# Optimization experiments

Measured on AMD Instinct MI355X. Metric: run time of the kernel, lower is better.

Reference implementation:

```python
import jax, jax.numpy as jnp
import numpy as np

N, IN_XC, IN_YC, OUTC, H, W = 8, 512, 256, 256, 96, 96
C2 = OUTC // 2  # 128
K = 3
NUM_LAT = K * K // 2 + 1  # 5


def conv2d(x, w, b=None, pad=0):
    out = jax.lax.conv_general_dilated(
        x, w, window_strides=(1, 1), padding=[(pad, pad), (pad, pad)],
        dimension_numbers=('NCHW', 'OIHW', 'NCHW'))
    if b is not None:
        out = out + b[None, :, None, None]
    return out


def patches3x3(x):
    # torch nn.Unfold(3, padding=1) taps, ordered (kh, kw) row-major -> [N,C,9,H,W]
    n, c, h, w = x.shape
    xp = jnp.pad(x, ((0, 0), (0, 0), (1, 1), (1, 1)))
    cols = [xp[:, :, i:i + h, j:j + w] for i in range(3) for j in range(3)]
    return jnp.stack(cols, axis=2)


def pool_to_3x3(x):
    # AdaptiveAvgPool2d(3) with H,W divisible by 3 == mean over equal bins
    n, c, h, w = x.shape
    return x.reshape(n, c, 3, h // 3, 3, w // 3).mean(axis=(3, 5))


def setup_inputs() -> dict:
    key = jax.random.key(0)
    ks = jax.random.split(key, 24)
    g = lambda i, shape, s=0.05: (jax.random.normal(ks[i], shape, dtype=jnp.float32) * s)
    return {
        'x': jax.random.normal(ks[0], (N, IN_XC, H, W), dtype=jnp.float32),
        'y': jax.random.normal(ks[1], (N, IN_YC, H, W), dtype=jnp.float32),
        # SDFM.down_input: 1x1 conv in_xC -> out_C
        'w_down': g(2, (OUTC, IN_XC, 1, 1)), 'b_down': g(3, (OUTC,)),
        # channel-attention MLP over 3x3 pooled grid
        'w_ce': g(4, (NUM_LAT, K * K)), 'w_gd': g(5, (K * K, NUM_LAT)),
        'bn_g': jnp.ones((C2,), jnp.float32), 'bn_b': jnp.zeros((C2,), jnp.float32),
        # gernerate_kernel_channel: 1x1 conv mid_in_yC -> mid_in_xC (both 128)
        'w_kc': g(6, (C2, C2, 1, 1)), 'b_kc': g(7, (C2,)),
        # gernerate_kernel_spatial: 3x3 conv C2->C2 then 1x1 conv C2->9
        'w_ks1': g(8, (C2, C2, 3, 3)), 'b_ks1': g(9, (C2,)),
        'w_ks2': g(10, (K * K, C2, 1, 1)), 'b_ks2': g(11, (K * K,)),
        # spatial-attention convs (bias=False)
        'w_sp1': g(12, (1, C2, 3, 3)), 'w_sp': g(13, (1, 2, 3, 3)),
        # branch fuse: 3x3 conv out_C -> out_C
        'w_fb': g(14, (OUTC, 2 * C2, 3, 3)), 'b_fb': g(15, (OUTC,)),
        # SDFM.fuse (BasicConv_PRelu): 3x3 conv 2*out_C -> out_C, BN(eval), PReLU
        'w_fuse': g(16, (OUTC, 2 * OUTC, 3, 3)),
        'bn2_g': jnp.ones((OUTC,), jnp.float32), 'bn2_b': jnp.zeros((OUTC,), jnp.float32),
        'prelu_a': jnp.full((OUTC,), 0.25, jnp.float32),
    }


def reference(x, y, w_down, b_down, w_ce, w_gd, bn_g, bn_b, w_kc, b_kc,
              w_ks1, b_ks1, w_ks2, b_ks2, w_sp1, w_sp, w_fb, b_fb,
              w_fuse, bn2_g, bn2_b, prelu_a):
    # SDFM.down_input
    x = conv2d(x, w_down, b_down, pad=0)          # [N, 256, H, W]
    n, c, h, w = x.shape
    c2 = c // 2
    x1, x2 = x[:, :c2], x[:, c2:]                 # [N,128,H,W] each
    y1, y2 = y[:, :c2], y[:, c2:]

    # --- channel branch: per-(sample,channel) dynamic 3x3 depthwise kernel ---
    gl = pool_to_3x3(x1).reshape(n, c2, K * K)    # [N,128,9]
    att = gl @ w_ce.T                              # ce (no bias) -> [N,128,5]
    att = att * bn_g[None, :, None] + bn_b[None, :, None]  # BN1d eval (rm=0, rv=1)
    att = jax.nn.relu(att)
    att = jax.nn.sigmoid(att @ w_gd.T)            # [N,128,9]

    kc = conv2d(pool_to_3x3(y1), w_kc, b_kc, pad=0)  # [N,128,3,3]
    kc = kc.reshape(n, c2, K * K) * att           # [N,128,9]
    # grouped conv (groups = N*C/2) == per-sample depthwise dynamic conv
    channel_after = jnp.einsum('nckhw,nck->nchw', patches3x3(x1), kc)

    # --- spatial branch: per-pixel dynamic 3x3 kernel ---
    ks = conv2d(conv2d(y2, w_ks1, b_ks1, pad=1), w_ks2, b_ks2, pad=0)  # [N,9,H,W]

    ksp = conv2d(x2, w_sp1, None, pad=1)          # [N,1,H,W]
    p = patches3x3(ksp).reshape(n, K * K, h, w)   # [N,9,H,W]
    avg = p.mean(axis=1, keepdims=True)
    mx = p.max(axis=1, keepdims=True)
    sp = jax.nn.sigmoid(conv2d(jnp.concatenate([avg, mx], axis=1), w_sp, None, pad=1))  # [N,1,H,W]

    kernel_after = (ks * sp).transpose(0, 2, 3, 1)[..., None]  # [N,H,W,9,1]

    # faithful replication of the original quirky reshape of unfold output:
    # [N, C2*9, H*W] -> [N, H, W, C2, 9]
    unfold_x = patches3x3(x2).reshape(n, c2 * K * K, h * w).reshape(n, h, w, c2, K * K)
    spatial_after = jnp.matmul(unfold_x, kernel_after)[..., 0]  # [N,H,W,C2]
    spatial_after = spatial_after.transpose(0, 3, 1, 2)          # [N,C2,H,W]

    result = jnp.concatenate([channel_after, spatial_after], axis=1)  # [N,256,H,W]
    r1 = conv2d(result, w_fb, b_fb, pad=1)        # branch fuse 3x3

    # SDFM.fuse: BasicConv_PRelu = conv3x3 (no bias) + BN(eval, rm=0,rv=1) + PReLU
    o = conv2d(jnp.concatenate([x, r1], axis=1), w_fuse, None, pad=1)
    o = o * bn2_g[None, :, None, None] + bn2_b[None, :, None, None]
    o = jnp.where(o >= 0, o, prelu_a[None, :, None, None] * o)
    return o
```

## Files before the change

kernel.cpp:

```cpp
#include <hip/hip_runtime.h>
#include <hip/hip_bf16.h>
#include <math.h>

#define HW 9216
#define IMG 96

typedef __bf16 bf16x8 __attribute__((ext_vector_type(8)));
typedef float  f32x4  __attribute__((ext_vector_type(4)));

__device__ __forceinline__ void gload16(const void* g, void* l) {
    __builtin_amdgcn_global_load_lds((const unsigned int*)g, (unsigned int*)l, 16, 0, 0);
}

#define WAITVN(N) asm volatile("s_waitcnt vmcnt(" #N ")" ::: "memory")
#define BARX()    { asm volatile("" ::: "memory"); __builtin_amdgcn_s_barrier(); asm volatile("" ::: "memory"); }

__global__ __launch_bounds__(256) void nchw2nhwc_kernel(
    const float* __restrict__ src, long n_stride_src,
    __hip_bfloat16* __restrict__ dst, int dst_stride)
{
    __shared__ float tile[32][65];
    const int px0 = blockIdx.x * 64;
    const int c0  = blockIdx.y * 32;
    const int n   = blockIdx.z;
    const int tid = threadIdx.x;
    const int tx = tid & 63, ty = tid >> 6;
    #pragma unroll
    for (int i = 0; i < 8; ++i)
        tile[ty + i * 4][tx] = src[n * n_stride_src + (long)(c0 + ty + i * 4) * HW + px0 + tx];
    __syncthreads();
    const int ci = tid & 31, pxl = tid >> 5;
    #pragma unroll
    for (int j = 0; j < 8; ++j) {
        int px = pxl + j * 8;
        dst[((long)n * HW + px0 + px) * dst_stride + c0 + ci] = __float2bfloat16(tile[ci][px]);
    }
}

__global__ __launch_bounds__(256) void wconv_kernel(
    const float* __restrict__ src, __hip_bfloat16* __restrict__ dst,
    int cout, int cin, int taps)
{
    int idx = blockIdx.x * 256 + threadIdx.x;
    if (idx >= cout * cin) return;
    int co = idx / cin, ci = idx % cin;
    for (int t = 0; t < taps; ++t)
        dst[((long)t * cout + co) * cin + ci] = __float2bfloat16(src[(long)idx * taps + t]);
}

template<int CIN, int TAPS, bool SPLIT>
__global__ __launch_bounds__(512, 1) void mfma_conv(
    const __hip_bfloat16* __restrict__ in_a,
    const __hip_bfloat16* __restrict__ in_b,
    const __hip_bfloat16* __restrict__ w_t,
    const float* __restrict__ bias,
    float* __restrict__ out_nchw, long nchw_nstride,
    __hip_bfloat16* __restrict__ out_nhwc, int nhwc_stride,
    int cout,
    const float* __restrict__ bng, const float* __restrict__ bnb,
    const float* __restrict__ pra,
    const __hip_bfloat16* __restrict__ zeropage)
{
    constexpr int ROWS = (TAPS == 9) ? 10 : 8;
    constexpr int COLS = (TAPS == 9) ? 98 : 96;
    constexpr int HOFF = (TAPS == 9) ? 1 : 0;
    constexpr int PSTR = SPLIT ? 256 : CIN;
    constexpr int NSEG_IN = ROWS * COLS * 4;
    constexpr int NSEG_W  = TAPS * 32 * 4;
    constexpr int IN_BYTES = NSEG_IN * 16;
    constexpr int BUF = IN_BYTES + NSEG_W * 16;
    constexpr int NCHUNK = CIN / 32;
    constexpr int FULL_IN = NSEG_IN / 512;
    constexpr int IN_TAIL = NSEG_IN % 512;
    constexpr int FULL_W  = NSEG_W / 512;
    constexpr int W_TAIL  = NSEG_W % 512;
    constexpr int IT_IN = FULL_IN + (IN_TAIL ? 1 : 0);
    constexpr int IT_W  = FULL_W + (W_TAIL ? 1 : 0);

    extern __shared__ __align__(16) char lds[];

    const int h0   = blockIdx.x * 8;
    const int cob  = blockIdx.y * 32;
    const int n    = blockIdx.z;
    const int tid  = threadIdx.x;
    const int lane = tid & 63;
    const int wave = tid >> 6;
    const int l16  = lane & 15, lg = lane >> 4;

    const long dAB = SPLIT ? ((const char*)in_b - (const char*)in_a - 448) : 0;

    const char* inptr[IT_IN];
    int inval[IT_IN];
    #pragma unroll
    for (int t = 0; t < IT_IN; ++t) {
        int seg = tid + t * 512;
        int s2 = (seg < NSEG_IN) ? seg : 0;
        int pix = s2 >> 2, qp = s2 & 3;
        int r = pix / COLS, c = pix % COLS;
        int h = h0 + r - HOFF, w = c - HOFF;
        int q = qp ^ ((c >> 1) & 3);
        bool valid = (h >= 0 && h < IMG && w >= 0 && w < IMG);
        inptr[t] = valid
            ? (const char*)(in_a + ((long)n * HW + h * IMG + w) * PSTR + q * 8)
            : (const char*)zeropage;
        inval[t] = valid ? 1 : 0;
    }
    const char* wptr[IT_W];
    #pragma unroll
    for (int t = 0; t < IT_W; ++t) {
        int seg = tid + t * 512;
        int s2 = (seg < NSEG_W) ? seg : 0;
        int tap = s2 >> 7, rem = s2 & 127;
        int co = rem >> 2, qp = rem & 3;
        int q = qp ^ ((co >> 1) & 3);
        wptr[t] = (const char*)(w_t + ((long)tap * cout + cob + co) * CIN + q * 8);
    }

    auto stage = [&](int bb, long adv) {
        char* ib = lds + bb * BUF;
        char* wb = ib + IN_BYTES;
        #pragma unroll
        for (int t = 0; t < FULL_IN; ++t) {
            gload16(inptr[t], ib + (tid + t * 512) * 16);
            if (inval[t]) inptr[t] += adv;
        }
        if (IN_TAIL) {
            if (tid < IN_TAIL) {
                gload16(inptr[IT_IN - 1], ib + (tid + FULL_IN * 512) * 16);
                if (inval[IT_IN - 1]) inptr[IT_IN - 1] += adv;
            }
        }
        #pragma unroll
        for (int t = 0; t < FULL_W; ++t) {
            gload16(wptr[t], wb + (tid + t * 512) * 16);
            wptr[t] += 64;
        }
        if (W_TAIL) {
            if (tid < W_TAIL) {
                gload16(wptr[IT_W - 1], wb + (tid + FULL_W * 512) * 16);
                wptr[IT_W - 1] += 64;
            }
        }
    };

    f32x4 acc[2][6];
    #pragma unroll
    for (int m = 0; m < 2; ++m)
        #pragma unroll
        for (int nf = 0; nf < 6; ++nf) acc[m][nf] = (f32x4){0.f, 0.f, 0.f, 0.f};

    const int qa = lg ^ ((l16 >> 1) & 3);
    const int a_off = l16 * 64 + qa * 16;

    stage(0, 64);
    WAITVN(0); BARX();

    for (int ch = 0; ch < NCHUNK; ++ch) {
        if (ch + 1 < NCHUNK) {
            long adv = (SPLIT && (ch + 1) == 7) ? dAB : 64;
            stage((ch + 1) & 1, adv);
            if constexpr (TAPS == 9) {
                if (wave < 2) { WAITVN(11); } else if (wave < 6) { WAITVN(10); } else { WAITVN(9); }
            } else {
                if (wave < 2) { WAITVN(7); } else { WAITVN(6); }
            }
        } else {
            WAITVN(0);
        }
        BARX();

        const char* ib = lds + (ch & 1) * BUF;
        const char* wb = ib + IN_BYTES;
        __builtin_amdgcn_s_setprio(1);
        #pragma unroll
        for (int tap = 0; tap < TAPS; ++tap) {
            const int g = (TAPS == 9) ? tap / 3 : 0;
            const int kx = (TAPS == 9) ? tap % 3 : 0;
            bf16x8 a0 = *(const bf16x8*)(wb + tap * 2048 + a_off);
            bf16x8 a1 = *(const bf16x8*)(wb + tap * 2048 + 1024 + a_off);
            #pragma unroll
            for (int nf = 0; nf < 6; ++nf) {
                const int c = nf * 16 + l16 + kx;
                const int qb = lg ^ ((c >> 1) & 3);
                bf16x8 b = *(const bf16x8*)(ib + ((wave + g) * COLS + c) * 64 + qb * 16);
                acc[0][nf] = __builtin_amdgcn_mfma_f32_16x16x32_bf16(a0, b, acc[0][nf], 0, 0, 0);
                acc[1][nf] = __builtin_amdgcn_mfma_f32_16x16x32_bf16(a1, b, acc[1][nf], 0, 0, 0);
            }
        }
        __builtin_amdgcn_s_setprio(0);
        BARX();
    }

    const int hrow = h0 + wave;
    #pragma unroll
    for (int m = 0; m < 2; ++m) {
        const int co = cob + m * 16 + lg * 4;
        float bs[4], g4[4], b4[4], p4[4];
        #pragma unroll
        for (int r = 0; r < 4; ++r) bs[r] = bias ? bias[co + r] : 0.f;
        if (bng) {
            #pragma unroll
            for (int r = 0; r < 4; ++r) { g4[r] = bng[co + r]; b4[r] = bnb[co + r]; p4[r] = pra[co + r]; }
        }
        #pragma unroll
        for (int nf = 0; nf < 6; ++nf) {
            const int wcol = nf * 16 + l16;
            const long px = (long)hrow * IMG + wcol;
            float v[4];
            #pragma unroll
            for (int r = 0; r < 4; ++r) {
                v[r] = acc[m][nf][r] + bs[r];
                if (bng) {
                    v[r] = v[r] * g4[r] + b4[r];
                    v[r] = (v[r] >= 0.f) ? v[r] : p4[r] * v[r];
                }
            }
            if (out_nchw) {
                #pragma unroll
                for (int r = 0; r < 4; ++r)
                    out_nchw[(long)n * nchw_nstride + (long)(co + r) * HW + px] = v[r];
            }
            if (out_nhwc) {
                union { __hip_bfloat16 h[4]; uint2 u; } pk;
                #pragma unroll
                for (int r = 0; r < 4; ++r) pk.h[r] = __float2bfloat16(v[r]);
                *reinterpret_cast<uint2*>(&out_nhwc[((long)n * HW + px) * nhwc_stride + co]) = pk.u;
            }
        }
    }
}

__global__ __launch_bounds__(256) void pool_kernel(
    const float* __restrict__ xd, const float* __restrict__ y,
    float* __restrict__ gl, float* __restrict__ py)
{
    const int c = blockIdx.x, n = blockIdx.y, which = blockIdx.z;
    const int tid = threadIdx.x;
    const float* src = (which == 0) ? (xd + ((long)n * 256 + c) * HW)
                                    : (y  + ((long)n * 256 + c) * HW);
    float local[9];
    #pragma unroll
    for (int k = 0; k < 9; ++k) local[k] = 0.f;
    for (int i = tid; i < HW; i += 256) {
        int h = i / 96, w = i % 96;
        local[(h / 32) * 3 + (w / 32)] += src[i];
    }
    __shared__ float red[9][4];
    const int wv = tid >> 6, lane = tid & 63;
    #pragma unroll
    for (int k = 0; k < 9; ++k) {
        float v = local[k];
        for (int off = 32; off > 0; off >>= 1) v += __shfl_down(v, off, 64);
        if (lane == 0) red[k][wv] = v;
    }
    __syncthreads();
    if (tid < 9) {
        float s = (red[tid][0] + red[tid][1] + red[tid][2] + red[tid][3]) * (1.f / 1024.f);
        float* dst = (which == 0) ? gl : py;
        dst[((long)n * 128 + c) * 9 + tid] = s;
    }
}

__global__ __launch_bounds__(128) void attkc_kernel(
    const float* __restrict__ gl, const float* __restrict__ py,
    const float* __restrict__ w_ce, const float* __restrict__ w_gd,
    const float* __restrict__ bng, const float* __restrict__ bnb,
    const float* __restrict__ w_kc, const float* __restrict__ b_kc,
    float* __restrict__ kc)
{
    const int n = blockIdx.x, c = threadIdx.x;
    __shared__ float py_s[128][9];
    #pragma unroll
    for (int k = 0; k < 9; ++k) py_s[c][k] = py[((long)n * 128 + c) * 9 + k];
    __syncthreads();
    float g[9];
    #pragma unroll
    for (int k = 0; k < 9; ++k) g[k] = gl[((long)n * 128 + c) * 9 + k];
    float t[5];
    #pragma unroll
    for (int l = 0; l < 5; ++l) {
        float s = 0.f;
        #pragma unroll
        for (int k = 0; k < 9; ++k) s += g[k] * w_ce[l * 9 + k];
        s = s * bng[c] + bnb[c];
        t[l] = s > 0.f ? s : 0.f;
    }
    float att[9];
    #pragma unroll
    for (int k = 0; k < 9; ++k) {
        float s = 0.f;
        #pragma unroll
        for (int l = 0; l < 5; ++l) s += t[l] * w_gd[k * 5 + l];
        att[k] = 1.f / (1.f + expf(-s));
    }
    float kc0[9];
    float bk = b_kc[c];
    #pragma unroll
    for (int k = 0; k < 9; ++k) kc0[k] = bk;
    for (int c2 = 0; c2 < 128; ++c2) {
        float wv = w_kc[c * 128 + c2];
        #pragma unroll
        for (int k = 0; k < 9; ++k) kc0[k] += wv * py_s[c2][k];
    }
    #pragma unroll
    for (int k = 0; k < 9; ++k)
        kc[((long)n * 128 + c) * 9 + k] = kc0[k] * att[k];
}

__global__ __launch_bounds__(256) void channel_nhwc_kernel(
    const __hip_bfloat16* __restrict__ catx, const float* __restrict__ kc,
    __hip_bfloat16* __restrict__ catfb)
{
    const int h  = blockIdx.x;
    const int n  = blockIdx.y;
    const int cg = (threadIdx.x & 15) * 8;
    const int w0 = threadIdx.x >> 4;
    float k9[8][9];
    #pragma unroll
    for (int j = 0; j < 8; ++j)
        #pragma unroll
        for (int t = 0; t < 9; ++t) k9[j][t] = kc[((long)n * 128 + cg + j) * 9 + t];
    const long pbase = (long)n * HW;
    for (int it = 0; it < 6; ++it) {
        const int w = w0 + it * 16;
        float acc[8];
        #pragma unroll
        for (int j = 0; j < 8; ++j) acc[j] = 0.f;
        #pragma unroll
        for (int ky = 0; ky < 3; ++ky) {
            const int hh = h + ky - 1;
            if (hh < 0 || hh >= IMG) continue;
            #pragma unroll
            for (int kx = 0; kx < 3; ++kx) {
                const int ww = w + kx - 1;
                if (ww < 0 || ww >= IMG) continue;
                bf16x8 v = *reinterpret_cast<const bf16x8*>(
                    &catx[(pbase + hh * IMG + ww) * 256 + cg]);
                #pragma unroll
                for (int j = 0; j < 8; ++j)
                    acc[j] += k9[j][ky * 3 + kx] * (float)v[j];
            }
        }
        union { __hip_bfloat16 hh[8]; uint4 u; } pk;
        #pragma unroll
        for (int j = 0; j < 8; ++j) pk.hh[j] = __float2bfloat16(acc[j]);
        *reinterpret_cast<uint4*>(&catfb[(pbase + h * IMG + w) * 256 + cg]) = pk.u;
    }
}

__global__ __launch_bounds__(256) void ks_kernel(
    const float* __restrict__ ksmid, const float* __restrict__ w_ks2,
    const float* __restrict__ b_ks2, float* __restrict__ ks)
{
    __shared__ float w_s[9 * 128];
    const int tid = threadIdx.x;
    for (int i = tid; i < 1152; i += 256) w_s[i] = w_ks2[i];
    __syncthreads();
    const int p = blockIdx.x * 256 + tid;
    const int n = blockIdx.y;
    float acc[9];
    #pragma unroll
    for (int k = 0; k < 9; ++k) acc[k] = b_ks2[k];
    for (int c = 0; c < 128; ++c) {
        float v = ksmid[((long)n * 128 + c) * HW + p];
        #pragma unroll
        for (int k = 0; k < 9; ++k) acc[k] += w_s[k * 128 + c] * v;
    }
    #pragma unroll
    for (int k = 0; k < 9; ++k) ks[((long)n * 9 + k) * HW + p] = acc[k];
}

__global__ __launch_bounds__(256) void ksp_nhwc_kernel(
    const __hip_bfloat16* __restrict__ catx, const float* __restrict__ w_sp1,
    float* __restrict__ ksp)
{
    __shared__ float w_s[9][128];
    const int tid = threadIdx.x;
    for (int i = tid; i < 1152; i += 256) {
        int ci = i / 9, tap = i % 9;
        w_s[tap][ci] = w_sp1[i];
    }
    __syncthreads();
    const int p = blockIdx.x * 256 + tid;
    const int n = blockIdx.y;
    const int h = p / 96, w = p % 96;
    const long pbase = (long)n * HW;
    float acc = 0.f;
    #pragma unroll
    for (int ky = 0; ky < 3; ++ky) {
        const int hh = h + ky - 1;
        if (hh < 0 || hh >= IMG) continue;
        #pragma unroll
        for (int kx = 0; kx < 3; ++kx) {
            const int ww = w + kx - 1;
            if (ww < 0 || ww >= IMG) continue;
            const int tap = ky * 3 + kx;
            const __hip_bfloat16* row = &catx[(pbase + hh * IMG + ww) * 256 + 128];
            #pragma unroll
            for (int vq = 0; vq < 16; ++vq) {
                bf16x8 v = *reinterpret_cast<const bf16x8*>(&row[vq * 8]);
                #pragma unroll
                for (int j = 0; j < 8; ++j)
                    acc += w_s[tap][vq * 8 + j] * (float)v[j];
            }
        }
    }
    ksp[pbase + p] = acc;
}

__global__ __launch_bounds__(256) void sp_kernel(
    const float* __restrict__ ksp, const float* __restrict__ w_sp,
    float* __restrict__ sp)
{
    const int p = blockIdx.x * 256 + threadIdx.x;
    const int n = blockIdx.y;
    const int h = p / 96, w = p % 96;
    const float* kp = ksp + (long)n * HW;
    float acc = 0.f;
    #pragma unroll
    for (int dy = 0; dy < 3; ++dy)
        #pragma unroll
        for (int dx = 0; dx < 3; ++dx) {
            int hh = h + dy - 1, ww = w + dx - 1;
            if (hh < 0 || hh >= 96 || ww < 0 || ww >= 96) continue;
            float s = 0.f, m = -1e30f;
            #pragma unroll
            for (int iy = 0; iy < 3; ++iy)
                #pragma unroll
                for (int ix = 0; ix < 3; ++ix) {
                    int h2 = hh + iy - 1, w2 = ww + ix - 1;
                    float v = (h2 >= 0 && h2 < 96 && w2 >= 0 && w2 < 96) ? kp[h2 * 96 + w2] : 0.f;
                    s += v; m = fmaxf(m, v);
                }
            acc += w_sp[dy * 3 + dx] * (s * (1.f / 9.f)) + w_sp[9 + dy * 3 + dx] * m;
        }
    sp[(long)n * HW + p] = 1.f / (1.f + expf(-acc));
}

__global__ __launch_bounds__(256) void spatial_kernel(
    const float* __restrict__ xd, const float* __restrict__ ks,
    const float* __restrict__ sp, __hip_bfloat16* __restrict__ catfb)
{
    const int cc = blockIdx.x;
    const int n  = blockIdx.y;
    const int tid = threadIdx.x;
    __shared__ float plane[HW];
    const float* src = xd + ((long)n * 256 + 128 + cc) * HW;
    for (int i = tid; i < HW / 4; i += 256)
        *reinterpret_cast<float4*>(&plane[i * 4]) = *reinterpret_cast<const float4*>(&src[i * 4]);
    __syncthreads();
    const int c  = tid & 127;
    const int pr = tid >> 7;
    const int c9 = c * 9;
    for (int j = 0; j < 36; ++j) {
        const int pl = pr + j * 2;
        const int p  = cc * 72 + pl;
        float spv = sp[(long)n * HW + p];
        float kv[9];
        #pragma unroll
        for (int k = 0; k < 9; ++k) kv[k] = ks[((long)n * 9 + k) * HW + p] * spv;
        const int base = pl * 1152 + c9;
        int kk0 = base / 9216;
        int r20 = base - kk0 * 9216;
        int h20 = r20 / 96;
        int w20 = r20 - h20 * 96;
        float acc = 0.f;
        #pragma unroll
        for (int k = 0; k < 9; ++k) {
            int kk = kk0, h2 = h20, w2 = w20 + k;
            if (w2 >= 96) { h2 += 1; w2 -= 96; }
            if (h2 >= 96) { kk += 1; h2 -= 96; }
            int hh = h2 + kk / 3 - 1;
            int ww = w2 + kk % 3 - 1;
            float v = (hh >= 0 && hh < 96 && ww >= 0 && ww < 96) ? plane[hh * 96 + ww] : 0.f;
            acc += v * kv[k];
        }
        catfb[((long)n * HW + p) * 256 + 128 + c] = __float2bfloat16(acc);
    }
}

extern "C" void kernel_launch(void* const* d_in, const int* in_sizes, int n_in,
                              void* d_out, int out_size, void* d_ws, size_t ws_size,
                              hipStream_t stream)
{
    const float* x      = (const float*)d_in[0];
    const float* y      = (const float*)d_in[1];
    const float* w_down = (const float*)d_in[2];
    const float* b_down = (const float*)d_in[3];
    const float* w_ce   = (const float*)d_in[4];
    const float* w_gd   = (const float*)d_in[5];
    const float* bn_g   = (const float*)d_in[6];
    const float* bn_b   = (const float*)d_in[7];
    const float* w_kc   = (const float*)d_in[8];
    const float* b_kc   = (const float*)d_in[9];
    const float* w_ks1  = (const float*)d_in[10];
    const float* b_ks1  = (const float*)d_in[11];
    const float* w_ks2  = (const float*)d_in[12];
    const float* b_ks2  = (const float*)d_in[13];
    const float* w_sp1  = (const float*)d_in[14];
    const float* w_sp   = (const float*)d_in[15];
    const float* w_fb   = (const float*)d_in[16];
    const float* b_fb   = (const float*)d_in[17];
    const float* w_fuse = (const float*)d_in[18];
    const float* bn2_g  = (const float*)d_in[19];
    const float* bn2_b  = (const float*)d_in[20];
    const float* prelu  = (const float*)d_in[21];
    float* out = (float*)d_out;
    char* ws = (char*)d_ws;

    const long HWl = HW;
    float* xd = (float*)ws;                               ws += 8L * 256 * HWl * 4;
    char* region2 = ws;                                   ws += 8L * HWl * 512 * 2;
    __hip_bfloat16* x_t    = (__hip_bfloat16*)region2;
    __hip_bfloat16* cat_r1 = (__hip_bfloat16*)region2;
    float*          ksmid  = (float*)region2;
    __hip_bfloat16* catfb  = (__hip_bfloat16*)(region2 + 8L * HWl * 256 * 2);
    __hip_bfloat16* cat_x  = (__hip_bfloat16*)ws;         ws += 8L * HWl * 256 * 2;
    __hip_bfloat16* y2t    = (__hip_bfloat16*)ws;         ws += 8L * HWl * 128 * 2;
    __hip_bfloat16* wdown_bf = (__hip_bfloat16*)ws;       ws += 1L * 256 * 512 * 2;
    __hip_bfloat16* wks1_bf  = (__hip_bfloat16*)ws;       ws += 9L * 128 * 128 * 2;
    __hip_bfloat16* wfb_bf   = (__hip_bfloat16*)ws;       ws += 9L * 256 * 256 * 2;
    __hip_bfloat16* wfuse_bf = (__hip_bfloat16*)ws;       ws += 9L * 256 * 512 * 2;
    float* ks   = (float*)ws;  ws += 8L * 9 * HWl * 4;
    float* ksp  = (float*)ws;  ws += 8L * HWl * 4;
    float* spb  = (float*)ws;  ws += 8L * HWl * 4;
    float* gl   = (float*)ws;  ws += 8L * 128 * 9 * 4;
    float* py   = (float*)ws;  ws += 8L * 128 * 9 * 4;
    float* kc   = (float*)ws;  ws += 8L * 128 * 9 * 4;
    __hip_bfloat16* zp = (__hip_bfloat16*)ws;  ws += 256;

    (void)hipMemsetAsync((void*)zp, 0, 256, stream);

    wconv_kernel<<<dim3(512), 256, 0, stream>>>(w_down, wdown_bf, 256, 512, 1);
    wconv_kernel<<<dim3(64),  256, 0, stream>>>(w_ks1,  wks1_bf,  128, 128, 9);
    wconv_kernel<<<dim3(256), 256, 0, stream>>>(w_fb,   wfb_bf,   256, 256, 9);
    wconv_kernel<<<dim3(512), 256, 0, stream>>>(w_fuse, wfuse_bf, 256, 512, 9);

    nchw2nhwc_kernel<<<dim3(144, 16, 8), 256, 0, stream>>>(x, 512L * HWl, x_t, 512);
    mfma_conv<512, 1, false><<<dim3(12, 8, 8), 512, 102400, stream>>>(
        x_t, nullptr, wdown_bf, b_down, xd, 256L * HWl, cat_x, 256, 256,
        nullptr, nullptr, nullptr, zp);

    nchw2nhwc_kernel<<<dim3(144, 4, 8), 256, 0, stream>>>(y + 128L * HWl, 256L * HWl, y2t, 128);

    pool_kernel<<<dim3(128, 8, 2), 256, 0, stream>>>(xd, y, gl, py);
    attkc_kernel<<<dim3(8), 128, 0, stream>>>(gl, py, w_ce, w_gd, bn_g, bn_b, w_kc, b_kc, kc);

    mfma_conv<128, 9, false><<<dim3(12, 4, 8), 512, 162304, stream>>>(
        y2t, nullptr, wks1_bf, b_ks1, ksmid, 128L * HWl, nullptr, 0, 128,
        nullptr, nullptr, nullptr, zp);
    ks_kernel<<<dim3(36, 8), 256, 0, stream>>>(ksmid, w_ks2, b_ks2, ks);

    ksp_nhwc_kernel<<<dim3(36, 8), 256, 0, stream>>>(cat_x, w_sp1, ksp);
    sp_kernel<<<dim3(36, 8), 256, 0, stream>>>(ksp, w_sp, spb);

    spatial_kernel<<<dim3(128, 8), 256, 0, stream>>>(xd, ks, spb, catfb);
    channel_nhwc_kernel<<<dim3(96, 8), 256, 0, stream>>>(cat_x, kc, catfb);

    mfma_conv<256, 9, false><<<dim3(12, 8, 8), 512, 162304, stream>>>(
        catfb, nullptr, wfb_bf, b_fb, nullptr, 0, cat_r1, 256, 256,
        nullptr, nullptr, nullptr, zp);

    mfma_conv<512, 9, true><<<dim3(12, 8, 8), 512, 162304, stream>>>(
        cat_x, cat_r1, wfuse_bf, nullptr, out, 256L * HWl, nullptr, 0, 256,
        bn2_g, bn2_b, prelu, zp);
}
```

Before: 671.6 us.

## Switch conv kernel to 32x32x16 MFMA with smaller blocks and two-per-CU occupancy

The implicit-GEMM conv kernel moves from 16x16x32 to 32x32x16 bf16 MFMA. Each block now handles 4 output rows by 64 output channels with 256 threads, and launch bounds allow two blocks per CU. The LDS layout changes from the XOR-swizzled layout to a grouped-by-8-pixel slot layout, and the K chunk shrinks to 16 or 32 channels, so the pipeline has more stages with smaller stages. The goals are more reuse per MFMA, fewer LDS bytes per block, and overlap between co-resident blocks. The risks are more halo rows per output row, more barriers, and possible LDS bank conflicts without the swizzle.

```diff
diff --git a/kernel.cpp b/kernel.cpp
--- a/kernel.cpp
+++ b/kernel.cpp
@@ -7,6 +7,7 @@
 
 typedef __bf16 bf16x8 __attribute__((ext_vector_type(8)));
 typedef float  f32x4  __attribute__((ext_vector_type(4)));
+typedef float  f32x16 __attribute__((ext_vector_type(16)));
 
 __device__ __forceinline__ void gload16(const void* g, void* l) {
     __builtin_amdgcn_global_load_lds((const unsigned int*)g, (unsigned int*)l, 16, 0, 0);
@@ -49,7 +50,7 @@
 }
 
 template<int CIN, int TAPS, bool SPLIT>
-__global__ __launch_bounds__(512, 1) void mfma_conv(
+__global__ __launch_bounds__(256, 2) void mfma_conv(
     const __hip_bfloat16* __restrict__ in_a,
     const __hip_bfloat16* __restrict__ in_b,
     const __hip_bfloat16* __restrict__ w_t,
@@ -61,45 +62,58 @@
     const float* __restrict__ pra,
     const __hip_bfloat16* __restrict__ zeropage)
 {
-    constexpr int ROWS = (TAPS == 9) ? 10 : 8;
+    constexpr int KSTEPS = (TAPS == 1) ? 2 : 1;
+    constexpr int QD     = 2 * KSTEPS;
+    constexpr int CICH   = 16 * KSTEPS;
+    constexpr int ROWS = (TAPS == 9) ? 6 : 4;
     constexpr int COLS = (TAPS == 9) ? 98 : 96;
     constexpr int HOFF = (TAPS == 9) ? 1 : 0;
     constexpr int PSTR = SPLIT ? 256 : CIN;
-    constexpr int NSEG_IN = ROWS * COLS * 4;
-    constexpr int NSEG_W  = TAPS * 32 * 4;
-    constexpr int IN_BYTES = NSEG_IN * 16;
-    constexpr int BUF = IN_BYTES + NSEG_W * 16;
-    constexpr int NCHUNK = CIN / 32;
-    constexpr int FULL_IN = NSEG_IN / 512;
-    constexpr int IN_TAIL = NSEG_IN % 512;
-    constexpr int FULL_W  = NSEG_W / 512;
-    constexpr int W_TAIL  = NSEG_W % 512;
-    constexpr int IT_IN = FULL_IN + (IN_TAIL ? 1 : 0);
-    constexpr int IT_W  = FULL_W + (W_TAIL ? 1 : 0);
+    constexpr int GP        = (COLS + 7) / 8;
+    constexpr int ROWSLOTS  = GP * 8 * QD;
+    constexpr int IN_SLOTS  = ROWS * ROWSLOTS;
+    constexpr int IN_BYTES  = IN_SLOTS * 16;
+    constexpr int WTAP      = 64 * QD;
+    constexpr int W_SLOTS   = TAPS * WTAP;
+    constexpr int BUF       = IN_BYTES + W_SLOTS * 16;
+    constexpr int NCHUNK    = CIN / CICH;
+    constexpr int FULL_IN = IN_SLOTS / 256;
+    constexpr int IN_TAIL = IN_SLOTS % 256;
+    constexpr int IT_IN   = FULL_IN + (IN_TAIL ? 1 : 0);
+    constexpr int FULL_W  = W_SLOTS / 256;
+    constexpr int W_TAIL  = W_SLOTS % 256;
+    constexpr int IT_W    = FULL_W + (W_TAIL ? 1 : 0);
+    constexpr int CROSS   = 256 / CICH;
+    constexpr long ADV    = 2 * CICH;
 
     extern __shared__ __align__(16) char lds[];
 
-    const int h0   = blockIdx.x * 8;
-    const int cob  = blockIdx.y * 32;
+    const int h0   = blockIdx.x * 4;
+    const int cob  = blockIdx.y * 64;
     const int n    = blockIdx.z;
     const int tid  = threadIdx.x;
     const int lane = tid & 63;
     const int wave = tid >> 6;
-    const int l16  = lane & 15, lg = lane >> 4;
-
-    const long dAB = SPLIT ? ((const char*)in_b - (const char*)in_a - 448) : 0;
+    const int l31  = lane & 31;
+    const int lq   = lane >> 5;
+    const int g3   = l31 >> 3, c7 = l31 & 7;
+
+    const long dAB = SPLIT ? ((const char*)in_b - (const char*)in_a - (CROSS - 1) * ADV) : 0;
 
     const char* inptr[IT_IN];
     int inval[IT_IN];
     #pragma unroll
     for (int t = 0; t < IT_IN; ++t) {
-        int seg = tid + t * 512;
-        int s2 = (seg < NSEG_IN) ? seg : 0;
-        int pix = s2 >> 2, qp = s2 & 3;
-        int r = pix / COLS, c = pix % COLS;
-        int h = h0 + r - HOFF, w = c - HOFF;
-        int q = qp ^ ((c >> 1) & 3);
-        bool valid = (h >= 0 && h < IMG && w >= 0 && w < IMG);
+        int seg = tid + t * 256;
+        int s2 = (seg < IN_SLOTS) ? seg : 0;
+        int r  = s2 / ROWSLOTS;
+        int sl = s2 - r * ROWSLOTS;
+        int g8 = sl / (8 * QD);
+        int rem = sl - g8 * 8 * QD;
+        int q  = rem >> 3, p7 = rem & 7;
+        int px = g8 * 8 + p7;
+        int h = h0 + r - HOFF, w = px - HOFF;
+        bool valid = (px < COLS) && (h >= 0 && h < IMG && w >= 0 && w < IMG);
         inptr[t] = valid
             ? (const char*)(in_a + ((long)n * HW + h * IMG + w) * PSTR + q * 8)
             : (const char*)zeropage;
@@ -108,11 +122,14 @@
     const char* wptr[IT_W];
     #pragma unroll
     for (int t = 0; t < IT_W; ++t) {
-        int seg = tid + t * 512;
-        int s2 = (seg < NSEG_W) ? seg : 0;
-        int tap = s2 >> 7, rem = s2 & 127;
-        int co = rem >> 2, qp = rem & 3;
-        int q = qp ^ ((co >> 1) & 3);
+        int seg = tid + t * 256;
+        int s2 = (seg < W_SLOTS) ? seg : 0;
+        int tap = s2 / WTAP;
+        int sl  = s2 - tap * WTAP;
+        int g8 = sl / (8 * QD);
+        int rem = sl - g8 * 8 * QD;
+        int q  = rem >> 3, p7 = rem & 7;
+        int co = g8 * 8 + p7;
         wptr[t] = (const char*)(w_t + ((long)tap * cout + cob + co) * CIN + q * 8);
     }
 
@@ -121,48 +138,47 @@
         char* wb = ib + IN_BYTES;
         #pragma unroll
         for (int t = 0; t < FULL_IN; ++t) {
-            gload16(inptr[t], ib + (tid + t * 512) * 16);
+            gload16(inptr[t], ib + (tid + t * 256) * 16);
             if (inval[t]) inptr[t] += adv;
         }
         if (IN_TAIL) {
             if (tid < IN_TAIL) {
-                gload16(inptr[IT_IN - 1], ib + (tid + FULL_IN * 512) * 16);
+                gload16(inptr[IT_IN - 1], ib + (tid + FULL_IN * 256) * 16);
                 if (inval[IT_IN - 1]) inptr[IT_IN - 1] += adv;
             }
         }
         #pragma unroll
         for (int t = 0; t < FULL_W; ++t) {
-            gload16(wptr[t], wb + (tid + t * 512) * 16);
-            wptr[t] += 64;
+            gload16(wptr[t], wb + (tid + t * 256) * 16);
+            wptr[t] += ADV;
         }
         if (W_TAIL) {
             if (tid < W_TAIL) {
-                gload16(wptr[IT_W - 1], wb + (tid + FULL_W * 512) * 16);
-                wptr[IT_W - 1] += 64;
+                gload16(wptr[IT_W - 1], wb + (tid + FULL_W * 256) * 16);
+                wptr[IT_W - 1] += ADV;
             }
         }
     };
 
-    f32x4 acc[2][6];
-    #pragma unroll
-    for (int m = 0; m < 2; ++m)
-        #pragma unroll
-        for (int nf = 0; nf < 6; ++nf) acc[m][nf] = (f32x4){0.f, 0.f, 0.f, 0.f};
-
-    const int qa = lg ^ ((l16 >> 1) & 3);
-    const int a_off = l16 * 64 + qa * 16;
-
-    stage(0, 64);
+    f32x16 acc[2][3];
+    #pragma unroll
+    for (int mf = 0; mf < 2; ++mf)
+        #pragma unroll
+        for (int nf = 0; nf < 3; ++nf)
+            #pragma unroll
+            for (int e = 0; e < 16; ++e) acc[mf][nf][e] = 0.f;
+
+    stage(0, ADV);
     WAITVN(0); BARX();
 
     for (int ch = 0; ch < NCHUNK; ++ch) {
         if (ch + 1 < NCHUNK) {
-            long adv = (SPLIT && (ch + 1) == 7) ? dAB : 64;
+            long adv = (SPLIT && (ch + 2) == CROSS) ? dAB : ADV;
             stage((ch + 1) & 1, adv);
             if constexpr (TAPS == 9) {
-                if (wave < 2) { WAITVN(11); } else if (wave < 6) { WAITVN(10); } else { WAITVN(9); }
+                if (wave < 2) { WAITVN(10); } else { WAITVN(9); }
             } else {
-                if (wave < 2) { WAITVN(7); } else { WAITVN(6); }
+                WAITVN(7);
             }
         } else {
             WAITVN(0);
@@ -171,60 +187,68 @@
 
         const char* ib = lds + (ch & 1) * BUF;
         const char* wb = ib + IN_BYTES;
+        const int rowbase = wave;
         __builtin_amdgcn_s_setprio(1);
         #pragma unroll
         for (int tap = 0; tap < TAPS; ++tap) {
-            const int g = (TAPS == 9) ? tap / 3 : 0;
+            const int g  = (TAPS == 9) ? tap / 3 : 0;
             const int kx = (TAPS == 9) ? tap % 3 : 0;
-            bf16x8 a0 = *(const bf16x8*)(wb + tap * 2048 + a_off);
-            bf16x8 a1 = *(const bf16x8*)(wb + tap * 2048 + 1024 + a_off);
-            #pragma unroll
-            for (int nf = 0; nf < 6; ++nf) {
-                const int c = nf * 16 + l16 + kx;
-                const int qb = lg ^ ((c >> 1) & 3);
-                bf16x8 b = *(const bf16x8*)(ib + ((wave + g) * COLS + c) * 64 + qb * 16);
-                acc[0][nf] = __builtin_amdgcn_mfma_f32_16x16x32_bf16(a0, b, acc[0][nf], 0, 0, 0);
-                acc[1][nf] = __builtin_amdgcn_mfma_f32_16x16x32_bf16(a1, b, acc[1][nf], 0, 0, 0);
+            #pragma unroll
+            for (int ks = 0; ks < KSTEPS; ++ks) {
+                const int q = ks * 2 + lq;
+                bf16x8 a0 = *(const bf16x8*)(wb + (tap * WTAP + ((g3)     * QD + q) * 8 + c7) * 16);
+                bf16x8 a1 = *(const bf16x8*)(wb + (tap * WTAP + ((4 + g3) * QD + q) * 8 + c7) * 16);
+                #pragma unroll
+                for (int nf = 0; nf < 3; ++nf) {
+                    const int px = nf * 32 + kx + l31;
+                    const int slot = ((px >> 3) * QD + q) * 8 + (px & 7);
+                    bf16x8 b = *(const bf16x8*)(ib + ((rowbase + g) * ROWSLOTS + slot) * 16);
+                    acc[0][nf] = __builtin_amdgcn_mfma_f32_32x32x16_bf16(a0, b, acc[0][nf], 0, 0, 0);
+                    acc[1][nf] = __builtin_amdgcn_mfma_f32_32x32x16_bf16(a1, b, acc[1][nf], 0, 0, 0);
+                }
             }
         }
         __builtin_amdgcn_s_setprio(0);
         BARX();
     }
 
-    const int hrow = h0 + wave;
-    #pragma unroll
-    for (int m = 0; m < 2; ++m) {
-        const int co = cob + m * 16 + lg * 4;
-        float bs[4], g4[4], b4[4], p4[4];
-        #pragma unroll
-        for (int r = 0; r < 4; ++r) bs[r] = bias ? bias[co + r] : 0.f;
-        if (bng) {
-            #pragma unroll
-            for (int r = 0; r < 4; ++r) { g4[r] = bng[co + r]; b4[r] = bnb[co + r]; p4[r] = pra[co + r]; }
-        }
-        #pragma unroll
-        for (int nf = 0; nf < 6; ++nf) {
-            const int wcol = nf * 16 + l16;
-            const long px = (long)hrow * IMG + wcol;
-            float v[4];
-            #pragma unroll
-            for (int r = 0; r < 4; ++r) {
-                v[r] = acc[m][nf][r] + bs[r];
-                if (bng) {
-                    v[r] = v[r] * g4[r] + b4[r];
-                    v[r] = (v[r] >= 0.f) ? v[r] : p4[r] * v[r];
+    const int row = h0 + wave;
+    #pragma unroll
+    for (int mf = 0; mf < 2; ++mf) {
+        #pragma unroll
+        for (int rr = 0; rr < 4; ++rr) {
+            const int co = cob + mf * 32 + rr * 8 + lq * 4;
+            float bs[4], g4[4], b4[4], p4[4];
+            #pragma unroll
+            for (int j = 0; j < 4; ++j) bs[j] = bias ? bias[co + j] : 0.f;
+            if (bng) {
+                #pragma unroll
+                for (int j = 0; j < 4; ++j) { g4[j] = bng[co + j]; b4[j] = bnb[co + j]; p4[j] = pra[co + j]; }
+            }
+            #pragma unroll
+            for (int nf = 0; nf < 3; ++nf) {
+                const int px = nf * 32 + l31;
+                const long pix = (long)row * IMG + px;
+                float v[4];
+                #pragma unroll
+                for (int j = 0; j < 4; ++j) {
+                    v[j] = acc[mf][nf][rr * 4 + j] + bs[j];
+                    if (bng) {
+                        v[j] = v[j] * g4[j] + b4[j];
+                        v[j] = (v[j] >= 0.f) ? v[j] : p4[j] * v[j];
+                    }
                 }
-            }
-            if (out_nchw) {
-                #pragma unroll
-                for (int r = 0; r < 4; ++r)
-                    out_nchw[(long)n * nchw_nstride + (long)(co + r) * HW + px] = v[r];
-            }
-            if (out_nhwc) {
-                union { __hip_bfloat16 h[4]; uint2 u; } pk;
-                #pragma unroll
-                for (int r = 0; r < 4; ++r) pk.h[r] = __float2bfloat16(v[r]);
-                *reinterpret_cast<uint2*>(&out_nhwc[((long)n * HW + px) * nhwc_stride + co]) = pk.u;
+                if (out_nchw) {
+                    #pragma unroll
+                    for (int j = 0; j < 4; ++j)
+                        out_nchw[(long)n * nchw_nstride + (long)(co + j) * HW + pix] = v[j];
+                }
+                if (out_nhwc) {
+                    union { __hip_bfloat16 h[4]; uint2 u; } pk;
+                    #pragma unroll
+                    for (int j = 0; j < 4; ++j) pk.h[j] = __float2bfloat16(v[j]);
+                    *reinterpret_cast<uint2*>(&out_nhwc[((long)n * HW + pix) * nhwc_stride + co]) = pk.u;
+                }
             }
         }
     }
@@ -537,7 +561,7 @@
     wconv_kernel<<<dim3(512), 256, 0, stream>>>(w_fuse, wfuse_bf, 256, 512, 9);
 
     nchw2nhwc_kernel<<<dim3(144, 16, 8), 256, 0, stream>>>(x, 512L * HWl, x_t, 512);
-    mfma_conv<512, 1, false><<<dim3(12, 8, 8), 512, 102400, stream>>>(
+    mfma_conv<512, 1, false><<<dim3(24, 4, 8), 256, 57344, stream>>>(
         x_t, nullptr, wdown_bf, b_down, xd, 256L * HWl, cat_x, 256, 256,
         nullptr, nullptr, nullptr, zp);
 
@@ -546,7 +570,7 @@
     pool_kernel<<<dim3(128, 8, 2), 256, 0, stream>>>(xd, y, gl, py);
     attkc_kernel<<<dim3(8), 128, 0, stream>>>(gl, py, w_ce, w_gd, bn_g, bn_b, w_kc, b_kc, kc);
 
-    mfma_conv<128, 9, false><<<dim3(12, 4, 8), 512, 162304, stream>>>(
+    mfma_conv<128, 9, false><<<dim3(24, 2, 8), 256, 76800, stream>>>(
         y2t, nullptr, wks1_bf, b_ks1, ksmid, 128L * HWl, nullptr, 0, 128,
         nullptr, nullptr, nullptr, zp);
     ks_kernel<<<dim3(36, 8), 256, 0, stream>>>(ksmid, w_ks2, b_ks2, ks);
@@ -557,11 +581,11 @@
     spatial_kernel<<<dim3(128, 8), 256, 0, stream>>>(xd, ks, spb, catfb);
     channel_nhwc_kernel<<<dim3(96, 8), 256, 0, stream>>>(cat_x, kc, catfb);
 
-    mfma_conv<256, 9, false><<<dim3(12, 8, 8), 512, 162304, stream>>>(
+    mfma_conv<256, 9, false><<<dim3(24, 4, 8), 256, 76800, stream>>>(
         catfb, nullptr, wfb_bf, b_fb, nullptr, 0, cat_r1, 256, 256,
         nullptr, nullptr, nullptr, zp);
 
-    mfma_conv<512, 9, true><<<dim3(12, 8, 8), 512, 162304, stream>>>(
+    mfma_conv<512, 9, true><<<dim3(24, 4, 8), 256, 76800, stream>>>(
         cat_x, cat_r1, wfuse_bf, nullptr, out, 256L * HWl, nullptr, 0, 256,
         bn2_g, bn2_b, prelu, zp);
 }
```

Result: slower. 695.8 us (+3.6%).
